# Optimization experiments

Measured on AMD Instinct MI355X. Metric: run time of the kernel, lower is better.

The kernel has to match this reference:

```python
import jax, jax.numpy as jnp
import numpy as np

B, S, D, H = 4, 2048, 1024, 16
HD = D // H
ROPE_THETA = 10000.0


def setup_inputs() -> dict:
    key = jax.random.key(0)
    ks = jax.random.split(key, 5)
    scale = 1.0 / np.sqrt(D)
    inp = {
        "x": jax.random.normal(ks[0], (B, S, D), dtype=jnp.float32),
        "Wq": jax.random.normal(ks[1], (D, D), dtype=jnp.float32) * scale,
        "bq": jnp.zeros((D,), jnp.float32),
        "Wk": jax.random.normal(ks[2], (D, D), dtype=jnp.float32) * scale,
        "bk": jnp.zeros((D,), jnp.float32),
        "Wv": jax.random.normal(ks[3], (D, D), dtype=jnp.float32) * scale,
        "bv": jnp.zeros((D,), jnp.float32),
        "Wo": jax.random.normal(ks[4], (D, D), dtype=jnp.float32) * scale,
        "bo": jnp.zeros((D,), jnp.float32),
        # causal mask: True means masked (j > i), matching masked_fill semantics
        "attn_mask": jnp.triu(jnp.ones((S, S), dtype=bool), k=1),
    }
    return inp


def _rope(x):
    # x: [B, H, S, HD]; half-split rotary embedding
    half = HD // 2
    inv_freq = 1.0 / (ROPE_THETA ** (jnp.arange(0, half, dtype=jnp.float32) / half))
    pos = jnp.arange(x.shape[2], dtype=jnp.float32)
    freqs = pos[:, None] * inv_freq[None, :]            # [S, half]
    cos = jnp.cos(freqs)[None, None]                    # [1,1,S,half]
    sin = jnp.sin(freqs)[None, None]
    x1, x2 = x[..., :half], x[..., half:]
    return jnp.concatenate([x1 * cos - x2 * sin, x2 * cos + x1 * sin], axis=-1)


def reference(x, Wq, bq, Wk, bk, Wv, bv, Wo, bo, attn_mask):
    def shape(t):  # [B,S,D] -> [B,H,S,HD]
        return t.reshape(B, S, H, HD).transpose(0, 2, 1, 3)

    q = shape(x @ Wq.T + bq)
    k = shape(x @ Wk.T + bk)
    v = shape(x @ Wv.T + bv)
    q = _rope(q)
    k = _rope(k)
    scores = jnp.einsum("bhqd,bhkd->bhqk", q, k) * (HD ** -0.5)
    scores = jnp.where(attn_mask[None, None], -jnp.inf, scores)
    w = jax.nn.softmax(scores, axis=-1)
    attn = jnp.einsum("bhqk,bhkd->bhqd", w, v)
    merged = attn.transpose(0, 2, 1, 3).reshape(B, S, D)
    return merged @ Wo.T + bo
```

## Files before the change

### kernel.cpp

```cpp
#include <hip/hip_runtime.h>
#include <math.h>

#define BATCH 4
#define SEQ   2048
#define DMODEL 1024
#define NHEAD 16
#define HDIM  64
#define MROWS (BATCH*SEQ)

typedef unsigned short u16;
typedef unsigned int   u32;

using bf16x8 = __attribute__((ext_vector_type(8))) short;
using f32x4  = __attribute__((ext_vector_type(4))) float;
using f32x16 = __attribute__((ext_vector_type(16))) float;

__device__ __forceinline__ u16 f2bf(float f) {
    u32 u = __float_as_uint(f);
    u += 0x7fffu + ((u >> 16) & 1u);
    return (u16)(u >> 16);
}
__device__ __forceinline__ u32 pack2bf(float a, float b) {
    u32 ua = __float_as_uint(a); ua += 0x7fffu + ((ua >> 16) & 1u);
    u32 ub = __float_as_uint(b); ub += 0x7fffu + ((ub >> 16) & 1u);
    return (ua >> 16) | (ub & 0xffff0000u);
}

#define GLOBAL_LOAD_LDS16(gp, lp)                                              \
    __builtin_amdgcn_global_load_lds(                                          \
        (const __attribute__((address_space(1))) void*)(gp),                   \
        (__attribute__((address_space(3))) void*)(lp), 16, 0, 0)

__global__ __launch_bounds__(256) void convert_inputs(
    const float* __restrict__ x,  const float* __restrict__ wq,
    const float* __restrict__ wk, const float* __restrict__ wv,
    const float* __restrict__ wo, u16* __restrict__ dst)
{
    long long i4 = ((long long)blockIdx.x * 256 + threadIdx.x) * 4;
    const float* src; long long off;
    if (i4 < 8388608LL) { src = x; off = i4; }
    else {
        long long j = i4 - 8388608LL;
        int seg = (int)(j >> 20);
        off = j & 1048575LL;
        src = (seg == 0) ? wq : (seg == 1) ? wk : (seg == 2) ? wv : wo;
    }
    float4 v = *(const float4*)(src + off);
    u32 lo = (u32)f2bf(v.x) | ((u32)f2bf(v.y) << 16);
    u32 hi = (u32)f2bf(v.z) | ((u32)f2bf(v.w) << 16);
    *(uint2*)(dst + i4) = make_uint2(lo, hi);
}

template<int QKV>
__global__ __launch_bounds__(256) void gemm_mfma(
    const u16* __restrict__ A,
    const u16* __restrict__ Wq_, const u16* __restrict__ Wk_, const u16* __restrict__ Wv_,
    const float* __restrict__ bq_, const float* __restrict__ bk_, const float* __restrict__ bv_,
    u16* __restrict__ Cq_, u16* __restrict__ Ck_, u16* __restrict__ Cv_,
    float* __restrict__ Cf)
{
    __shared__ u16 As[128 * 32];
    __shared__ u16 Ws[128 * 32];

    const int t    = threadIdx.x;
    const int lane = t & 63;
    const int w    = t >> 6;
    const int quad = lane >> 4;
    const int l15  = lane & 15;

    const int bx  = blockIdx.x;
    const int xcd = bx & 7;
    const int i_  = bx >> 3;
    const int bml = i_ & 7;
    const int n_  = (QKV ? ((i_ >> 3) & 7) : (i_ >> 3));
    const int seg = (QKV ? (i_ >> 6) : 0);

    const u16*   W    = (seg == 0) ? Wq_ : (seg == 1) ? Wk_ : Wv_;
    const float* bias = (seg == 0) ? bq_ : (seg == 1) ? bk_ : bv_;
    u16*         Cb   = (seg == 0) ? Cq_ : (seg == 1) ? Ck_ : Cv_;

    const int bm   = (xcd * 8 + bml) * 128;
    const int bn   = n_ * 128;
    const int wrow = (w & 1) * 64;
    const int wcol = (w >> 1) * 64;

    const int srl = lane >> 2;
    const int sc  = (lane & 3) ^ ((lane >> 3) & 3);

    f32x4 acc[4][4] = {};

    for (int k0 = 0; k0 < DMODEL; k0 += 32) {
        __syncthreads();
        #pragma unroll
        for (int i = 0; i < 2; i++) {
            int row = 32 * w + 16 * i + srl;
            GLOBAL_LOAD_LDS16(A + (size_t)(bm + row) * DMODEL + k0 + sc * 8,
                              &As[(32 * w + 16 * i) * 32]);
            GLOBAL_LOAD_LDS16(W + (size_t)(bn + row) * DMODEL + k0 + sc * 8,
                              &Ws[(32 * w + 16 * i) * 32]);
        }
        __syncthreads();

        bf16x8 af[4], bfr[4];
        const int pc = quad ^ ((l15 >> 1) & 3);
        #pragma unroll
        for (int i = 0; i < 4; i++)
            af[i] = *(const bf16x8*)&As[(wrow + 16 * i + l15) * 32 + pc * 8];
        #pragma unroll
        for (int j = 0; j < 4; j++)
            bfr[j] = *(const bf16x8*)&Ws[(wcol + 16 * j + l15) * 32 + pc * 8];
        #pragma unroll
        for (int i = 0; i < 4; i++)
            #pragma unroll
            for (int j = 0; j < 4; j++)
                acc[i][j] = __builtin_amdgcn_mfma_f32_16x16x32_bf16(af[i], bfr[j], acc[i][j], 0, 0, 0);
    }

    float bv[4];
    #pragma unroll
    for (int j = 0; j < 4; j++) bv[j] = bias[bn + wcol + 16 * j + l15];

    if constexpr (QKV == 0) {
        #pragma unroll
        for (int i = 0; i < 4; i++)
            #pragma unroll
            for (int r = 0; r < 4; r++) {
                int mg = bm + wrow + 16 * i + quad * 4 + r;
                #pragma unroll
                for (int j = 0; j < 4; j++)
                    Cf[(size_t)mg * DMODEL + bn + wcol + 16 * j + l15] = acc[i][j][r] + bv[j];
            }
    } else {
        if (seg == 2) {
            #pragma unroll
            for (int i = 0; i < 4; i++)
                #pragma unroll
                for (int r = 0; r < 4; r++) {
                    int mg = bm + wrow + 16 * i + quad * 4 + r;
                    #pragma unroll
                    for (int j = 0; j < 4; j++)
                        Cb[(size_t)mg * DMODEL + bn + wcol + 16 * j + l15] = f2bf(acc[i][j][r] + bv[j]);
                }
        } else {
            const float qscale = (seg == 0) ? 0.125f : 1.0f;
            float inv[2];
            #pragma unroll
            for (int j = 0; j < 2; j++) {
                int d = 16 * j + l15;
                inv[j] = exp2f(-(float)d * 0.4152410118609203f);
            }
            #pragma unroll
            for (int i = 0; i < 4; i++)
                #pragma unroll
                for (int r = 0; r < 4; r++) {
                    int mg = bm + wrow + 16 * i + quad * 4 + r;
                    int s  = mg & (SEQ - 1);
                    #pragma unroll
                    for (int j = 0; j < 2; j++) {
                        float f = (float)s * inv[j];
                        float sn, cs;
                        __sincosf(f, &sn, &cs);
                        float a1 = acc[i][j][r]     + bv[j];
                        float a2 = acc[i][j + 2][r] + bv[j + 2];
                        float o1 = (a1 * cs - a2 * sn) * qscale;
                        float o2 = (a2 * cs + a1 * sn) * qscale;
                        Cb[(size_t)mg * DMODEL + bn + wcol + 16 * j       + l15] = f2bf(o1);
                        Cb[(size_t)mg * DMODEL + bn + wcol + 16 * (j + 2) + l15] = f2bf(o2);
                    }
                }
        }
    }
}

__global__ __launch_bounds__(256) void attn_mfma(
    const u16* __restrict__ Q, const u16* __restrict__ K,
    const u16* __restrict__ V, u16* __restrict__ O)
{
    __shared__ u16 Qs[128 * 64];
    __shared__ u16 Ks[64 * 64];
    __shared__ u16 Vt[64 * 64];
    __shared__ u16 Ps[128 * 64];
    __shared__ float lS[128];

    const int t    = threadIdx.x;
    const int lane = t & 63;
    const int w    = t >> 6;
    const int l31  = lane & 31;
    const int hl   = lane >> 5;
    const int bid  = blockIdx.x;
    const int bh   = bid & 63;
    const int qt   = 15 - (bid >> 6);
    const int h    = bh & (NHEAD - 1);
    const int b    = bh >> 4;
    const int q0   = qt * 128;

    const size_t gbase = ((size_t)b * SEQ) * DMODEL + h * HDIM;

    {
        int rl = lane >> 3, cp = lane & 7;
        int c  = cp ^ rl;
        #pragma unroll
        for (int i = 0; i < 4; i++) {
            int row = 32 * w + 8 * i + rl;
            GLOBAL_LOAD_LDS16(Q + gbase + (size_t)(q0 + row) * DMODEL + c * 8,
                              &Qs[(32 * w + 8 * i) * 64]);
        }
    }
    __syncthreads();

    bf16x8 qf[4];
    {
        int row = 32 * w + l31;
        #pragma unroll
        for (int s = 0; s < 4; s++) {
            int c = (hl + 2 * s) ^ (row & 7);
            qf[s] = *(const bf16x8*)&Qs[row * 64 + c * 8];
        }
    }

    float lsum = 0.0f;
    f32x16 oacc[2] = {};

    const int ktn = 2 * qt + 2;
    for (int kt = 0; kt < ktn; kt++) {
        const int k0 = kt * 64;
        __syncthreads();

        {
            int rl = lane >> 3, cp = lane & 7;
            int c  = cp ^ rl;
            #pragma unroll
            for (int i = 0; i < 2; i++) {
                int row = 16 * w + 8 * i + rl;
                GLOBAL_LOAD_LDS16(K + gbase + (size_t)(k0 + row) * DMODEL + c * 8,
                                  &Ks[(16 * w + 8 * i) * 64]);
            }
        }
        {
            int j0 = (t & 31) * 2, d0 = (t >> 5) * 8;
            uint4 va = *(const uint4*)(V + gbase + (size_t)(k0 + j0)     * DMODEL + d0);
            uint4 vb = *(const uint4*)(V + gbase + (size_t)(k0 + j0 + 1) * DMODEL + d0);
            const u16* pa = (const u16*)&va;
            const u16* pb = (const u16*)&vb;
            int jd = t & 31, pos = jd & 3, ch = jd >> 2;
            #pragma unroll
            for (int e = 0; e < 8; e++) {
                int row = d0 + e;
                int pcch = ch ^ (row & 7);
                *(u32*)&Vt[row * 64 + pcch * 8 + pos * 2] = (u32)pa[e] | ((u32)pb[e] << 16);
            }
        }
        __syncthreads();

        const bool act = (k0 <= q0 + 32 * w + 31);
        if (act) {
            const int qrow = 32 * w + l31;
            const int qg   = q0 + qrow;
            #pragma unroll
            for (int krh = 0; krh < 2; krh++) {
                const bool qact = (k0 + 32 * krh <= q0 + 32 * w + 31);
                if (!qact) {
                    #pragma unroll
                    for (int g = 0; g < 4; g++)
                        #pragma unroll
                        for (int pp = 0; pp < 2; pp++) {
                            int kr = 32 * krh + 8 * g + 4 * hl + 2 * pp;
                            int jd = kr >> 1;
                            int pcc = (jd >> 2) ^ (qrow & 7);
                            *(u32*)&Ps[qrow * 64 + pcc * 8 + (jd & 3) * 2] = 0u;
                        }
                    continue;
                }
                f32x16 s = {};
                #pragma unroll
                for (int stp = 0; stp < 4; stp++) {
                    int row = 32 * krh + l31;
                    int c   = (hl + 2 * stp) ^ (l31 & 7);
                    bf16x8 ka = *(const bf16x8*)&Ks[row * 64 + c * 8];
                    s = __builtin_amdgcn_mfma_f32_32x32x16_bf16(ka, qf[stp], s, 0, 0, 0);
                }
                if (k0 + 32 * krh + 31 > q0 + 32 * w) {
                    #pragma unroll
                    for (int r = 0; r < 16; r++) {
                        int krg = k0 + 32 * krh + (r & 3) + 8 * (r >> 2) + 4 * hl;
                        if (krg > qg) s[r] = -1e30f;
                    }
                }
                float pv[16];
                #pragma unroll
                for (int r = 0; r < 16; r++) { pv[r] = __expf(s[r]); lsum += pv[r]; }
                #pragma unroll
                for (int g = 0; g < 4; g++)
                    #pragma unroll
                    for (int pp = 0; pp < 2; pp++) {
                        int kr = 32 * krh + 8 * g + 4 * hl + 2 * pp;
                        int jd = kr >> 1;
                        int pcc = (jd >> 2) ^ (qrow & 7);
                        *(u32*)&Ps[qrow * 64 + pcc * 8 + (jd & 3) * 2] =
                            pack2bf(pv[4 * g + 2 * pp], pv[4 * g + 2 * pp + 1]);
                    }
            }

            #pragma unroll
            for (int stp = 0; stp < 4; stp++) {
                int c = (hl + 2 * stp) ^ (l31 & 7);
                bf16x8 pf = *(const bf16x8*)&Ps[qrow * 64 + c * 8];
                #pragma unroll
                for (int dh = 0; dh < 2; dh++) {
                    bf16x8 vf = *(const bf16x8*)&Vt[(32 * dh + l31) * 64 + c * 8];
                    oacc[dh] = __builtin_amdgcn_mfma_f32_32x32x16_bf16(pf, vf, oacc[dh], 0, 0, 0);
                }
            }
        }
    }

    lsum += __shfl_xor(lsum, 32, 64);
    if (lane < 32) lS[32 * w + lane] = lsum;
    __syncthreads();

    #pragma unroll
    for (int g = 0; g < 4; g++) {
        f32x4 lv = *(const f32x4*)&lS[32 * w + 8 * g + 4 * hl];
        #pragma unroll
        for (int rr = 0; rr < 4; rr++) {
            int qg = q0 + 32 * w + rr + 8 * g + 4 * hl;
            float inv = 1.0f / lv[rr];
            #pragma unroll
            for (int dh = 0; dh < 2; dh++) {
                float o = oacc[dh][4 * g + rr] * inv;
                O[gbase + (size_t)qg * DMODEL + 32 * dh + l31] = f2bf(o);
            }
        }
    }
}

extern "C" void kernel_launch(void* const* d_in, const int* in_sizes, int n_in,
                              void* d_out, int out_size, void* d_ws, size_t ws_size,
                              hipStream_t stream)
{
    const float* x  = (const float*)d_in[0];
    const float* Wq = (const float*)d_in[1];
    const float* bq = (const float*)d_in[2];
    const float* Wk = (const float*)d_in[3];
    const float* bk = (const float*)d_in[4];
    const float* Wv = (const float*)d_in[5];
    const float* bv = (const float*)d_in[6];
    const float* Wo = (const float*)d_in[7];
    const float* bo = (const float*)d_in[8];

    u16* wsp = (u16*)d_ws;
    u16* xb  = wsp;
    u16* Wqb = wsp + 8388608;
    u16* Wkb = Wqb + 1048576;
    u16* Wvb = Wkb + 1048576;
    u16* Wob = Wvb + 1048576;
    u16* Qb  = Wob + 1048576;
    u16* Kb  = Qb + 8388608;
    u16* Vb  = Kb + 8388608;
    u16* Ab  = Vb + 8388608;

    convert_inputs<<<12288, 256, 0, stream>>>(x, Wq, Wk, Wv, Wo, xb);

    gemm_mfma<1><<<1536, 256, 0, stream>>>(xb, Wqb, Wkb, Wvb, bq, bk, bv,
                                           Qb, Kb, Vb, nullptr);

    attn_mfma<<<1024, 256, 0, stream>>>(Qb, Kb, Vb, Ab);

    gemm_mfma<0><<<512, 256, 0, stream>>>(Ab, Wob, nullptr, nullptr, bo, nullptr, nullptr,
                                          nullptr, nullptr, nullptr, (float*)d_out);
}
```

Baseline: 281.4 us.

## Triple-buffer GEMM with 256x128 tiles, BK=64 and interleaved async LDS loads

```diff
diff --git a/kernel.cpp b/kernel.cpp
--- a/kernel.cpp
+++ b/kernel.cpp
@@ -52,69 +52,115 @@
 }
 
 template<int QKV>
-__global__ __launch_bounds__(256) void gemm_mfma(
+__global__ __launch_bounds__(512) void gemm_mfma(
     const u16* __restrict__ A,
     const u16* __restrict__ Wq_, const u16* __restrict__ Wk_, const u16* __restrict__ Wv_,
     const float* __restrict__ bq_, const float* __restrict__ bk_, const float* __restrict__ bv_,
     u16* __restrict__ Cq_, u16* __restrict__ Ck_, u16* __restrict__ Cv_,
     float* __restrict__ Cf)
 {
-    __shared__ u16 As[128 * 32];
-    __shared__ u16 Ws[128 * 32];
+    __shared__ u16 As[3 * 256 * 64];
+    __shared__ u16 Ws[3 * 128 * 64];
 
     const int t    = threadIdx.x;
     const int lane = t & 63;
     const int w    = t >> 6;
     const int quad = lane >> 4;
     const int l15  = lane & 15;
+    const int wm   = w >> 1;
+    const int wn   = w & 1;
 
     const int bx  = blockIdx.x;
     const int xcd = bx & 7;
     const int i_  = bx >> 3;
-    const int bml = i_ & 7;
-    const int n_  = (QKV ? ((i_ >> 3) & 7) : (i_ >> 3));
-    const int seg = (QKV ? (i_ >> 6) : 0);
+    const int bml = i_ & 3;
+    const int n_  = i_ >> 2;
+    const int seg = (QKV ? (n_ >> 3) : 0);
+    const int nn  = (QKV ? (n_ & 7) : n_);
 
     const u16*   W    = (seg == 0) ? Wq_ : (seg == 1) ? Wk_ : Wv_;
     const float* bias = (seg == 0) ? bq_ : (seg == 1) ? bk_ : bv_;
     u16*         Cb   = (seg == 0) ? Cq_ : (seg == 1) ? Ck_ : Cv_;
 
-    const int bm   = (xcd * 8 + bml) * 128;
-    const int bn   = n_ * 128;
-    const int wrow = (w & 1) * 64;
-    const int wcol = (w >> 1) * 64;
-
-    const int srl = lane >> 2;
-    const int sc  = (lane & 3) ^ ((lane >> 3) & 3);
+    const int bm   = (xcd * 4 + bml) * 256;
+    const int bn   = nn * 128;
+    const int wrow = wm * 64;
+    const int wcol = wn * 64;
+
+    const int sr8 = lane >> 3;
+    const int scl = (lane & 7) ^ sr8;
+    const u16* gA = A + (size_t)(bm + 8 * w + sr8) * DMODEL + scl * 8;
+    const u16* gB = W + (size_t)(bn + 8 * w + sr8) * DMODEL + scl * 8;
+
+#define STAGE_A(li, kt, bs)                                                    \
+    GLOBAL_LOAD_LDS16(gA + (size_t)(li) * 64 * DMODEL + (kt) * 64,             \
+                      &As[(bs) * 16384 + ((li) * 64 + 8 * w) * 64])
+#define STAGE_B(li, kt, bs)                                                    \
+    GLOBAL_LOAD_LDS16(gB + (size_t)(li) * 64 * DMODEL + (kt) * 64,             \
+                      &Ws[(bs) * 8192 + ((li) * 64 + 8 * w) * 64])
+
+    STAGE_A(0, 0, 0); STAGE_A(1, 0, 0); STAGE_A(2, 0, 0); STAGE_A(3, 0, 0);
+    STAGE_B(0, 0, 0); STAGE_B(1, 0, 0);
+    STAGE_A(0, 1, 1); STAGE_A(1, 1, 1); STAGE_A(2, 1, 1); STAGE_A(3, 1, 1);
+    STAGE_B(0, 1, 1); STAGE_B(1, 1, 1);
+    asm volatile("s_waitcnt vmcnt(6)" ::: "memory");
+    __builtin_amdgcn_s_barrier();
+
+    const int c0 = (quad ^ (l15 & 7)) * 8;
+    const int c1 = c0 ^ 32;
 
     f32x4 acc[4][4] = {};
 
-    for (int k0 = 0; k0 < DMODEL; k0 += 32) {
-        __syncthreads();
-        #pragma unroll
-        for (int i = 0; i < 2; i++) {
-            int row = 32 * w + 16 * i + srl;
-            GLOBAL_LOAD_LDS16(A + (size_t)(bm + row) * DMODEL + k0 + sc * 8,
-                              &As[(32 * w + 16 * i) * 32]);
-            GLOBAL_LOAD_LDS16(W + (size_t)(bn + row) * DMODEL + k0 + sc * 8,
-                              &Ws[(32 * w + 16 * i) * 32]);
-        }
-        __syncthreads();
-
-        bf16x8 af[4], bfr[4];
-        const int pc = quad ^ ((l15 >> 1) & 3);
-        #pragma unroll
-        for (int i = 0; i < 4; i++)
-            af[i] = *(const bf16x8*)&As[(wrow + 16 * i + l15) * 32 + pc * 8];
-        #pragma unroll
-        for (int j = 0; j < 4; j++)
-            bfr[j] = *(const bf16x8*)&Ws[(wcol + 16 * j + l15) * 32 + pc * 8];
-        #pragma unroll
-        for (int i = 0; i < 4; i++)
-            #pragma unroll
-            for (int j = 0; j < 4; j++)
-                acc[i][j] = __builtin_amdgcn_mfma_f32_16x16x32_bf16(af[i], bfr[j], acc[i][j], 0, 0, 0);
-    }
+    int bsel = 0;
+    for (int kt = 0; kt < DMODEL / 64; ++kt) {
+        const u16* Ab = &As[bsel * 16384];
+        const u16* Bb = &Ws[bsel * 8192];
+        const int  ks = kt + 2;
+        const int  sb = (bsel >= 1) ? bsel - 1 : 2;
+        const bool st = (ks < DMODEL / 64);
+
+        bf16x8 af[4], bf[4];
+
+        #pragma unroll
+        for (int i = 0; i < 4; ++i)
+            af[i] = *(const bf16x8*)&Ab[(wrow + 16 * i + l15) * 64 + c0];
+        #pragma unroll
+        for (int j = 0; j < 4; ++j)
+            bf[j] = *(const bf16x8*)&Bb[(wcol + 16 * j + l15) * 64 + c0];
+        if (st) { STAGE_A(0, ks, sb); STAGE_A(1, ks, sb); STAGE_A(2, ks, sb); }
+        __builtin_amdgcn_s_barrier();
+        __builtin_amdgcn_s_setprio(1);
+        #pragma unroll
+        for (int i = 0; i < 4; ++i)
+            #pragma unroll
+            for (int j = 0; j < 4; ++j)
+                acc[i][j] = __builtin_amdgcn_mfma_f32_16x16x32_bf16(af[i], bf[j], acc[i][j], 0, 0, 0);
+        __builtin_amdgcn_s_setprio(0);
+        __builtin_amdgcn_s_barrier();
+
+        #pragma unroll
+        for (int i = 0; i < 4; ++i)
+            af[i] = *(const bf16x8*)&Ab[(wrow + 16 * i + l15) * 64 + c1];
+        #pragma unroll
+        for (int j = 0; j < 4; ++j)
+            bf[j] = *(const bf16x8*)&Bb[(wcol + 16 * j + l15) * 64 + c1];
+        if (st) { STAGE_A(3, ks, sb); STAGE_B(0, ks, sb); STAGE_B(1, ks, sb); }
+        __builtin_amdgcn_s_barrier();
+        __builtin_amdgcn_s_setprio(1);
+        #pragma unroll
+        for (int i = 0; i < 4; ++i)
+            #pragma unroll
+            for (int j = 0; j < 4; ++j)
+                acc[i][j] = __builtin_amdgcn_mfma_f32_16x16x32_bf16(af[i], bf[j], acc[i][j], 0, 0, 0);
+        __builtin_amdgcn_s_setprio(0);
+        if (st) asm volatile("s_waitcnt vmcnt(6)" ::: "memory");
+        else    asm volatile("s_waitcnt vmcnt(0)" ::: "memory");
+        __builtin_amdgcn_s_barrier();
+
+        bsel = (bsel == 2) ? 0 : bsel + 1;
+    }
+#undef STAGE_A
+#undef STAGE_B
 
     float bv[4];
     #pragma unroll
@@ -361,11 +407,11 @@
 
     convert_inputs<<<12288, 256, 0, stream>>>(x, Wq, Wk, Wv, Wo, xb);
 
-    gemm_mfma<1><<<1536, 256, 0, stream>>>(xb, Wqb, Wkb, Wvb, bq, bk, bv,
-                                           Qb, Kb, Vb, nullptr);
+    gemm_mfma<1><<<768, 512, 0, stream>>>(xb, Wqb, Wkb, Wvb, bq, bk, bv,
+                                          Qb, Kb, Vb, nullptr);
 
     attn_mfma<<<1024, 256, 0, stream>>>(Qb, Kb, Vb, Ab);
 
-    gemm_mfma<0><<<512, 256, 0, stream>>>(Ab, Wob, nullptr, nullptr, bo, nullptr, nullptr,
+    gemm_mfma<0><<<256, 512, 0, stream>>>(Ab, Wob, nullptr, nullptr, bo, nullptr, nullptr,
                                           nullptr, nullptr, nullptr, (float*)d_out);
 }
```

New measurement: 263.4 us. 6.4% less time.
